# Optimization experiments

Measured on AMD Instinct MI355X. Metric: run time of the kernel, lower is better.

The kernel has to match this reference:

```python
import jax, jax.numpy as jnp
import numpy as np

G = 4096   # num_genes
P = 4096   # num_perts
H = 64     # hidden_size
B = 4      # num_graphs
E1 = 81920 # coexpress edges
E2 = 81920 # GO edges
FF = 512   # transformer ffn
NH = 2     # attention heads
INTER, LAT = 32, 16  # VAE dims

def _bn(x, g, b, eps=1e-5):
    # BatchNorm1d in training mode: batch stats (biased var)
    m = x.mean(0); v = x.var(0)
    return (x - m) / jnp.sqrt(v + eps) * g + b

def _ln(x, g, b, eps=1e-5):
    m = x.mean(-1, keepdims=True); v = x.var(-1, keepdims=True)
    return (x - m) / jnp.sqrt(v + eps) * g + b

def _mlp2(x, w1, b1, g1, be1, w2, b2, g2, be2):
    # MLP([a,b,c]) builds Linear->BN->ReLU->Linear->BN (trailing ReLU stripped)
    h = jax.nn.relu(_bn(x @ w1.T + b1, g1, be1))
    return _bn(h @ w2.T + b2, g2, be2)

def _sgconv(x, ei, ew, w, b, n):
    # SGConv K=1: gcn_norm (self loops, symmetric norm) then linear
    src = jnp.concatenate([ei[0], jnp.arange(n)])
    dst = jnp.concatenate([ei[1], jnp.arange(n)])
    wgt = jnp.concatenate([ew, jnp.ones((n,), ew.dtype)])
    deg = jax.ops.segment_sum(wgt, dst, num_segments=n)
    dinv = jnp.where(deg > 0, 1.0 / jnp.sqrt(jnp.where(deg > 0, deg, 1.0)), 0.0)
    norm = dinv[dst] * wgt * dinv[src]
    agg = jax.ops.segment_sum(norm[:, None] * x[src], dst, num_segments=n)
    return agg @ w.T + b

def setup_inputs():
    ks = iter(jax.random.split(jax.random.key(0), 80))
    def nrm(shape, s=0.05):
        return jax.random.normal(next(ks), shape, dtype=jnp.float32) * s
    d = {}
    d['x'] = jax.random.uniform(next(ks), (B * G,), dtype=jnp.float32)
    d['pert_idx'] = jax.random.randint(next(ks), (B, 2), 0, P)
    d['mask'] = jnp.zeros((G, G), jnp.float32)
    d['ei_co'] = jax.random.randint(next(ks), (2, E1), 0, G)
    d['w_co'] = jax.random.uniform(next(ks), (E1,), dtype=jnp.float32)
    d['ei_go'] = jax.random.randint(next(ks), (2, E2), 0, P)
    d['w_go'] = jax.random.uniform(next(ks), (E2,), dtype=jnp.float32)
    d['gene_emb'] = nrm((G, H)); d['emb_pos'] = nrm((G, H)); d['pert_tbl'] = nrm((P, H))
    d['sg_co_w'] = nrm((H, H)); d['sg_co_b'] = jnp.zeros((H,))
    d['sg_go_w'] = nrm((H, H)); d['sg_go_b'] = jnp.zeros((H,))
    d['bn_emb_g'] = jnp.ones((H,)); d['bn_emb_b'] = jnp.zeros((H,))
    for pre, din, dout in [('etv2_1', H, H), ('etv2_2', H, H), ('pf_1', H, H), ('pf_2', H, H), ('rw_1', H, 2 * H), ('rw_2', 2 * H, H)]:
        d[pre + '_w'] = nrm((dout, din)); d[pre + '_b'] = jnp.zeros((dout,))
        d[pre + '_g'] = jnp.ones((dout,)); d[pre + '_be'] = jnp.zeros((dout,))
    d['bnpb_g'] = jnp.ones((H,)); d['bnpb_b'] = jnp.zeros((H,))
    d['attn_in_w'] = nrm((3 * H, H)); d['attn_in_b'] = jnp.zeros((3 * H,))
    d['attn_out_w'] = nrm((H, H)); d['attn_out_b'] = jnp.zeros((H,))
    d['ln1_g'] = jnp.ones((H,)); d['ln1_b'] = jnp.zeros((H,))
    d['ff1_w'] = nrm((FF, H)); d['ff1_b'] = jnp.zeros((FF,))
    d['ff2_w'] = nrm((H, FF)); d['ff2_b'] = jnp.zeros((H,))
    d['ln2_g'] = jnp.ones((H,)); d['ln2_b'] = jnp.zeros((H,))
    d['indv_w1'] = nrm((G, H)); d['indv_b1'] = jnp.zeros((G,))
    d['vae_e1_w'] = nrm((INTER, G)); d['vae_e1_b'] = jnp.zeros((INTER,))
    d['vae_mu_w'] = nrm((LAT, INTER)); d['vae_mu_b'] = jnp.zeros((LAT,))
    d['vae_lv_w'] = nrm((LAT, INTER)); d['vae_lv_b'] = jnp.zeros((LAT,))
    d['vae_d1_w'] = nrm((INTER, LAT)); d['vae_d1_b'] = jnp.zeros((INTER,))
    d['vae_d2_w'] = nrm((G, INTER)); d['vae_d2_b'] = jnp.zeros((G,))
    d['eps'] = jax.random.normal(next(ks), (B, LAT), dtype=jnp.float32)
    return d

def reference(x, pert_idx, mask, ei_co, w_co, ei_go, w_go, gene_emb, emb_pos, pert_tbl, sg_co_w, sg_co_b, sg_go_w, sg_go_b, bn_emb_g, bn_emb_b, etv2_1_w, etv2_1_b, etv2_1_g, etv2_1_be, etv2_2_w, etv2_2_b, etv2_2_g, etv2_2_be, pf_1_w, pf_1_b, pf_1_g, pf_1_be, pf_2_w, pf_2_b, pf_2_g, pf_2_be, rw_1_w, rw_1_b, rw_1_g, rw_1_be, rw_2_w, rw_2_b, rw_2_g, rw_2_be, bnpb_g, bnpb_b, attn_in_w, attn_in_b, attn_out_w, attn_out_b, ln1_g, ln1_b, ff1_w, ff1_b, ff2_w, ff2_b, ln2_g, ln2_b, indv_w1, indv_b1, vae_e1_w, vae_e1_b, vae_mu_w, vae_mu_b, vae_lv_w, vae_lv_b, vae_d1_w, vae_d1_b, vae_d2_w, vae_d2_b, eps):
    # gene base embedding (identical across graphs until pert fusion)
    base = jax.nn.relu(_bn(gene_emb, bn_emb_g, bn_emb_b))               # [G,H]
    pos = _sgconv(emb_pos, ei_co, w_co, sg_co_w, sg_co_b, G)            # 1 gene-GNN layer
    base = base + 0.2 * pos
    base = _mlp2(base, etv2_1_w, etv2_1_b, etv2_1_g, etv2_1_be, etv2_2_w, etv2_2_b, etv2_2_g, etv2_2_be)
    # pert embeddings propagated on GO graph
    pge = _sgconv(pert_tbl, ei_go, w_go, sg_go_w, sg_go_b, P)           # [P,H]
    # per-graph pert_track: sum of pert embeddings (all pert_idx valid)
    psum = pge[pert_idx].sum(axis=1)                                    # [B,H]
    etot = _mlp2(psum, pf_1_w, pf_1_b, pf_1_g, pf_1_be, pf_2_w, pf_2_b, pf_2_g, pf_2_be)
    base_b = base[None, :, :] + etot[:, None, :]                        # [B,G,H]
    flat = jax.nn.relu(_bn(base_b.reshape(B * G, H), bnpb_g, bnpb_b))
    out = _mlp2(flat, rw_1_w, rw_1_b, rw_1_g, rw_1_be, rw_2_w, rw_2_b, rw_2_g, rw_2_be)
    out = out.reshape(B, G, H)
    # transformer encoder layer (post-norm, relu, nhead=2), eval/no-dropout
    qkv = out @ attn_in_w.T + attn_in_b
    q, k, v = jnp.split(qkv, 3, axis=-1)
    hd = H // NH
    q = q.reshape(B, G, NH, hd); k = k.reshape(B, G, NH, hd); v = v.reshape(B, G, NH, hd)
    sc = jnp.einsum('bqhd,bkhd->bhqk', q, k) / np.float32(np.sqrt(hd)) + mask
    a = jax.nn.softmax(sc, axis=-1)
    ctx = jnp.einsum('bhqk,bkhd->bqhd', a, v).reshape(B, G, H)
    att = ctx @ attn_out_w.T + attn_out_b
    h1 = _ln(out + att, ln1_g, ln1_b)
    ff = jax.nn.relu(h1 @ ff1_w.T + ff1_b) @ ff2_w.T + ff2_b
    enc = _ln(h1 + ff, ln2_g, ln2_b)
    # per-gene linear: (enc.unsqueeze(-1)*indv_w1).sum(2)+indv_b1
    pred0 = jnp.einsum('bgh,gh->bg', enc, indv_w1) + indv_b1
    # VAE branch on raw expression
    xr = x.reshape(B, G)
    he = jax.nn.relu(xr @ vae_e1_w.T + vae_e1_b)
    mu = he @ vae_mu_w.T + vae_mu_b
    lv = he @ vae_lv_w.T + vae_lv_b
    z = mu + eps * jnp.exp(0.5 * lv)
    hdc = jax.nn.relu(z @ vae_d1_w.T + vae_d1_b)
    recon = hdc @ vae_d2_w.T + vae_d2_b
    kl = -0.5 * jnp.mean(jnp.sum(1.0 + lv - mu ** 2 - jnp.exp(lv), axis=1))
    recon = jnp.where(xr == 0, 0.0, recon)
    pred = pred0 + recon
    return (pred, kl)
```

## Files before the change

### kernel.cpp

```cpp
#include <hip/hip_runtime.h>
#include <hip/hip_bf16.h>
#include <math.h>

#define GG 4096
#define PP 4096
#define HH 64
#define BB 4
#define E1N 81920
#define E2N 81920
#define FFD 512
#define BNEPS 1e-5f
#define LOG2E 1.44269504088896341f
#define QPRE (0.17677669529663687f * LOG2E)

typedef unsigned short ushort_t;
typedef unsigned int uint_t;
using sh8 = __attribute__((ext_vector_type(8))) short;
using sh4 = __attribute__((ext_vector_type(4))) short;
using f4  = __attribute__((ext_vector_type(4))) float;

struct MaskOn  { static constexpr bool v = true; };
struct MaskOff { static constexpr bool v = false; };

#if __has_builtin(__builtin_amdgcn_mfma_f32_16x16x16bf16_1k)
#define MFMA16(a, b, c) __builtin_amdgcn_mfma_f32_16x16x16bf16_1k((a), (b), (c), 0, 0, 0)
#elif __has_builtin(__builtin_amdgcn_mfma_f32_16x16x16_bf16)
#define MFMA16(a, b, c) __builtin_amdgcn_mfma_f32_16x16x16_bf16((a), (b), (c), 0, 0, 0)
#else
static __device__ inline f4 mfma16_asm(sh4 a, sh4 b, f4 c) {
    f4 d;
    asm volatile("v_mfma_f32_16x16x16_bf16 %0, %1, %2, %3"
                 : "=v"(d) : "v"(a), "v"(b), "v"(c));
    return d;
}
#define MFMA16(a, b, c) mfma16_asm((a), (b), (c))
#endif

#define OF_STATS   0
#define OF_DEGCO   2048
#define OF_DEGGO   6144
#define OF_PSLOT   10240
#define OF_ETOT    10752
#define OF_HDC     11008
#define OF_HE      11136
#define OF_MFLAG   11264
#define OF_CNT     12288
#define OF_OFFS    16384
#define OF_WOFF    20608
#define OF_SSRC    24704
#define OF_SNRM    106624
#define OF_BASEIN  274432
#define OF_Y1      536576
#define OF_Y2      798720
#define OF_FLAT    1060864
#define OF_RW1     2109440
#define OF_RW2     4206592
#define OF_OUT     5255168
#define OF_QKV     6303744
#define OF_QB      12288
#define OF_KB      (OF_QB + 524288)
#define OF_VF      OF_FLAT
#define OF_OPA     OF_QKV
#define OF_OPB     OF_OUT
#define OF_LP      OF_RW1
#define OPS        1048576
#define OF_W1B     9449472
#define OF_W2B     9465856

__device__ inline ushort_t f2b(float f) {
    uint_t u = __builtin_bit_cast(uint_t, f);
    u += 0x7FFFu + ((u >> 16) & 1u);
    return (ushort_t)(u >> 16);
}

__device__ inline void gld16(const void* gptr, void* lptr) {
    __builtin_amdgcn_global_load_lds(
        (const __attribute__((address_space(1))) uint_t*)gptr,
        (__attribute__((address_space(3))) uint_t*)lptr, 16, 0, 0);
}

__device__ void dev_vae_he(int bid, const float* __restrict__ x, const float* __restrict__ W,
                           const float* __restrict__ bias, float* he, float* sh) {
    int b = bid >> 5, i = bid & 31;
    float s = 0.f;
    for (int g = threadIdx.x; g < 4096; g += 256) s += x[b * 4096 + g] * W[i * 4096 + g];
    sh[threadIdx.x] = s;
    __syncthreads();
    for (int o = 128; o > 0; o >>= 1) {
        if (threadIdx.x < o) sh[threadIdx.x] += sh[threadIdx.x + o];
        __syncthreads();
    }
    if (threadIdx.x == 0) he[b * 32 + i] = fmaxf(sh[0] + bias[i], 0.f);
}

__device__ void dev_vae_mid(const float* __restrict__ he,
                            const float* __restrict__ muw, const float* __restrict__ mub,
                            const float* __restrict__ lvw, const float* __restrict__ lvb,
                            const float* __restrict__ d1w, const float* __restrict__ d1b,
                            const float* __restrict__ eps, float* hdc, float* klout, float* zs) {
    int t = threadIdx.x;
    if (t < 64) {
        int b = t >> 4, l = t & 15;
        float mu = mub[l], lv = lvb[l];
        for (int i = 0; i < 32; i++) {
            float hv = he[b * 32 + i];
            mu += hv * muw[l * 32 + i];
            lv += hv * lvw[l * 32 + i];
        }
        zs[t] = mu + eps[t] * expf(0.5f * lv);
        float kterm = 1.f + lv - mu * mu - expf(lv);
        for (int o = 32; o > 0; o >>= 1) kterm += __shfl_xor(kterm, o, 64);
        if (t == 0) klout[0] = -0.5f * kterm * 0.25f;
    }
    __syncthreads();
    if (t < 128) {
        int b = t >> 5, i = t & 31;
        float a = d1b[i];
        for (int l = 0; l < 16; l++) a += zs[b * 16 + l] * d1w[i * 16 + l];
        hdc[t] = fmaxf(a, 0.f);
    }
}

__device__ void dev_edge_deg(int bid, const int* __restrict__ ei, const float* __restrict__ w,
                             float* deg, int E, int* cnt) {
    int e = bid * 256 + threadIdx.x;
    if (e < E) {
        int d = ei[E + e];
        atomicAdd(&deg[d], w[e]);
        if (cnt) atomicAdd(&cnt[d], 1);
    }
}

__device__ void dev_cs_part(int bid, const float* __restrict__ X, int N,
                            float* sum, float* sumsq, float* sh) {
    int t = threadIdx.x;
    int col = t & 63, ro = t >> 6;
    int rows = N >> 8;
    int r0 = bid * rows;
    float s = 0.f, q = 0.f;
    for (int r = r0 + ro; r < r0 + rows; r += 4) {
        float v = X[r * 64 + col];
        s += v; q += v * v;
    }
    float* ls = sh; float* lq = sh + 256;
    ls[t] = s; lq[t] = q;
    __syncthreads();
    if (t < 64) {
        for (int j = t + 64; j < 256; j += 64) { s += ls[j]; q += lq[j]; }
        atomicAdd(&sum[t], s);
        atomicAdd(&sumsq[t], q);
    }
}

__device__ void dev_mask_scan(int bid, const float* __restrict__ mask, int* flag) {
    const uint4* m4 = (const uint4*)mask;
    const int total = (GG * GG) / 4;
    uint_t acc = 0u;
    for (int i = bid * 256 + threadIdx.x; i < total; i += 512 * 256) {
        uint4 v = m4[i];
        acc |= v.x | v.y | v.z | v.w;
    }
    if (acc) atomicOr(flag, 1);
}

__device__ void dev_scatter(int bid, const int* __restrict__ ei, const float* __restrict__ w,
                            const float* __restrict__ deg,
                            int* woff, int* ssrc, float* snrm) {
    int e = bid * 256 + threadIdx.x;
    if (e >= E1N) return;
    int src = ei[e], dst = ei[E1N + e];
    float nrm = rsqrtf(deg[dst] + 1.f) * w[e] * rsqrtf(deg[src] + 1.f);
    int pos = atomicAdd(&woff[dst], 1);
    ssrc[pos] = src;
    snrm[pos] = nrm;
}

__device__ void dev_pert_edges(int bid, const int* __restrict__ pidx, const int* __restrict__ ei,
                               const float* __restrict__ w, const float* __restrict__ deg,
                               const float* __restrict__ tbl, float* pslot) {
    int e = bid * 256 + threadIdx.x;
    int lane = threadIdx.x & 63;
    bool valid = e < E2N;
    int dst = valid ? ei[E2N + e] : -1;
    int hit = 0;
    #pragma unroll
    for (int s = 0; s < 8; s++) hit |= (pidx[s] == dst) ? (1 << s) : 0;
    if (__ballot(hit != 0) == 0) return;
    int src = valid ? ei[e] : 0;
    float nrm = 0.f;
    if (hit) nrm = rsqrtf(deg[dst] + 1.f) * w[e] * rsqrtf(deg[src] + 1.f);
    for (int s = 0; s < 8; s++) {
        unsigned long long m = __ballot((hit >> s) & 1);
        while (m) {
            int l = __builtin_ctzll(m);
            m &= m - 1;
            int es = __shfl(src, l, 64);
            float en = __shfl(nrm, l, 64);
            atomicAdd(&pslot[s * 64 + lane], en * tbl[es * 64 + lane]);
        }
    }
}

__device__ void dev_base_combine(int bid, const float* __restrict__ gene_emb,
                                 const int* __restrict__ off, const int* __restrict__ ssrc,
                                 const float* __restrict__ snrm,
                                 const float* __restrict__ emb_pos,
                                 const float* __restrict__ deg,
                                 const float* __restrict__ W, const float* __restrict__ bias,
                                 const float* __restrict__ bsum, const float* __restrict__ bsq,
                                 const float* __restrict__ bg, const float* __restrict__ bb,
                                 float* out, float* sh) {
    float* Wt = sh;
    float* a = sh + 4160;
    int t = threadIdx.x;
    for (int i = t; i < 4096; i += 256) Wt[(i & 63) * 65 + (i >> 6)] = W[i];
    int rr = t >> 6, h = t & 63;
    int g = bid * 4 + rr;
    float acc = emb_pos[g * 64 + h] / (deg[g] + 1.f);
    int e = off[g];
    const int e1 = off[g + 1];
    for (; e + 4 <= e1; e += 4) {
        int s0 = ssrc[e], s1 = ssrc[e + 1], s2 = ssrc[e + 2], s3 = ssrc[e + 3];
        float n0 = snrm[e], n1 = snrm[e + 1], n2 = snrm[e + 2], n3 = snrm[e + 3];
        acc += n0 * emb_pos[s0 * 64 + h];
        acc += n1 * emb_pos[s1 * 64 + h];
        acc += n2 * emb_pos[s2 * 64 + h];
        acc += n3 * emb_pos[s3 * 64 + h];
    }
    for (; e < e1; e++) acc += snrm[e] * emb_pos[ssrc[e] * 64 + h];
    a[rr * 64 + h] = acc;
    __syncthreads();
    float y = bias[h];
    const float* ar = a + rr * 64;
    #pragma unroll 8
    for (int k = 0; k < 64; k++) y += ar[k] * Wt[k * 65 + h];
    const float invN = 1.0f / (float)GG;
    float m = bsum[h] * invN;
    float is_ = rsqrtf(bsq[h] * invN - m * m + BNEPS);
    float v = gene_emb[g * 64 + h];
    v = (v - m) * is_ * bg[h] + bb[h];
    v = fmaxf(v, 0.f);
    out[g * 64 + h] = v + 0.2f * y;
}

__device__ void dev_pert_mlp(const float* __restrict__ pslot, const int* __restrict__ pidx,
                             const float* __restrict__ deg, const float* __restrict__ tbl,
                             const float* __restrict__ gw, const float* __restrict__ gb,
                             const float* __restrict__ w1, const float* __restrict__ b1,
                             const float* __restrict__ g1, const float* __restrict__ be1,
                             const float* __restrict__ w2, const float* __restrict__ b2,
                             const float* __restrict__ g2, const float* __restrict__ be2,
                             float* etot, float* sh) {
    float* pge = sh;
    float* psum = sh + 512;
    float* y = sh + 768;
    float* mh = sh + 1024;
    float* ih = sh + 1088;
    int t = threadIdx.x;
    for (int j = t; j < 512; j += 256) {
        int s = j >> 6, h = j & 63;
        int n = pidx[s];
        float invd = 1.0f / (deg[n] + 1.f);
        float acc = gb[h];
        for (int k = 0; k < 64; k++)
            acc += (pslot[s * 64 + k] + tbl[n * 64 + k] * invd) * gw[h * 64 + k];
        pge[j] = acc;
    }
    __syncthreads();
    { int b = t >> 6, h = t & 63; psum[t] = pge[2 * b * 64 + h] + pge[(2 * b + 1) * 64 + h]; }
    __syncthreads();
    { int h = t & 63; int b = t >> 6;
      float acc = b1[h];
      for (int k = 0; k < 64; k++) acc += psum[b * 64 + k] * w1[h * 64 + k];
      y[t] = acc; }
    __syncthreads();
    if (t < 64) {
        float s = 0.f, sq = 0.f;
        for (int b = 0; b < 4; b++) { float v = y[b * 64 + t]; s += v; sq += v * v; }
        float m = s * 0.25f;
        mh[t] = m; ih[t] = rsqrtf(sq * 0.25f - m * m + BNEPS);
    }
    __syncthreads();
    { int h = t & 63;
      float v = (y[t] - mh[h]) * ih[h] * g1[h] + be1[h];
      psum[t] = fmaxf(v, 0.f); }
    __syncthreads();
    { int h = t & 63; int b = t >> 6;
      float acc = b2[h];
      for (int k = 0; k < 64; k++) acc += psum[b * 64 + k] * w2[h * 64 + k];
      y[t] = acc; }
    __syncthreads();
    if (t < 64) {
        float s = 0.f, sq = 0.f;
        for (int b = 0; b < 4; b++) { float v = y[b * 64 + t]; s += v; sq += v * v; }
        float m = s * 0.25f;
        mh[t] = m; ih[t] = rsqrtf(sq * 0.25f - m * m + BNEPS);
    }
    __syncthreads();
    { int h = t & 63;
      etot[t] = (y[t] - mh[h]) * ih[h] * g2[h] + be2[h]; }
}

__global__ void k_fat12(float* ws, const int* __restrict__ ei_co, const float* __restrict__ w_co,
                        const int* __restrict__ ei_go, const float* __restrict__ w_go,
                        const float* __restrict__ gene_emb, const float* __restrict__ x,
                        const float* __restrict__ ve1_w, const float* __restrict__ ve1_b,
                        const float* __restrict__ ff1_w, const float* __restrict__ ff2_w,
                        const float* __restrict__ mask) {
    __shared__ float sh[512];
    int bid = blockIdx.x;
    if (bid < 320) dev_edge_deg(bid, ei_co, w_co, ws + OF_DEGCO, E1N, (int*)(ws + OF_CNT));
    else if (bid < 640) dev_edge_deg(bid - 320, ei_go, w_go, ws + OF_DEGGO, E2N, nullptr);
    else if (bid < 896) dev_cs_part(bid - 640, gene_emb, GG, ws + OF_STATS, ws + OF_STATS + 128, sh);
    else if (bid < 1024) dev_vae_he(bid - 896, x, ve1_w, ve1_b, ws + OF_HE, sh);
    else if (bid < 1280) {
        int i = (bid - 1024) * 256 + threadIdx.x;
        ushort_t* W1b = (ushort_t*)(ws + OF_W1B);
        ushort_t* W2b = (ushort_t*)(ws + OF_W2B);
        if (i < 32768) W1b[i] = f2b(ff1_w[i]);
        else W2b[i - 32768] = f2b(ff2_w[i - 32768]);
    } else dev_mask_scan(bid - 1280, mask, (int*)(ws + OF_MFLAG));
}

__global__ void k_scan(float* ws) {
    int* cnt = (int*)(ws + OF_CNT);
    int* off = (int*)(ws + OF_OFFS);
    int* woff = (int*)(ws + OF_WOFF);
    __shared__ int part[256];
    const int t = threadIdx.x;
    int loc[16];
    int s = 0;
    #pragma unroll
    for (int i = 0; i < 16; i++) { loc[i] = s; s += cnt[t * 16 + i]; }
    part[t] = s;
    __syncthreads();
    for (int o = 1; o < 256; o <<= 1) {
        int v = (t >= o) ? part[t - o] : 0;
        __syncthreads();
        part[t] += v;
        __syncthreads();
    }
    int prev = (t == 0) ? 0 : part[t - 1];
    #pragma unroll
    for (int i = 0; i < 16; i++) {
        int o = prev + loc[i];
        off[t * 16 + i] = o;
        woff[t * 16 + i] = o;
    }
    if (t == 255) off[4096] = part[255];
}

__global__ void k_fat3(float* ws, const int* __restrict__ ei_co, const float* __restrict__ w_co,
                       const int* __restrict__ pidx,
                       const int* __restrict__ ei_go, const float* __restrict__ w_go,
                       const float* __restrict__ pert_tbl,
                       const float* __restrict__ vmu_w, const float* __restrict__ vmu_b,
                       const float* __restrict__ vlv_w, const float* __restrict__ vlv_b,
                       const float* __restrict__ vd1_w, const float* __restrict__ vd1_b,
                       const float* __restrict__ veps, float* klout) {
    __shared__ float sh[512];
    int bid = blockIdx.x;
    if (bid < 320)
        dev_scatter(bid, ei_co, w_co, ws + OF_DEGCO,
                    (int*)(ws + OF_WOFF), (int*)(ws + OF_SSRC), ws + OF_SNRM);
    else if (bid < 640)
        dev_pert_edges(bid - 320, pidx, ei_go, w_go, ws + OF_DEGGO, pert_tbl, ws + OF_PSLOT);
    else dev_vae_mid(ws + OF_HE, vmu_w, vmu_b, vlv_w, vlv_b, vd1_w, vd1_b, veps,
                     ws + OF_HDC, klout, sh);
}

__global__ void k_fat4(float* ws, const float* __restrict__ gene_emb,
                       const float* __restrict__ emb_pos,
                       const float* __restrict__ sg_co_w, const float* __restrict__ sg_co_b,
                       const float* __restrict__ bn_emb_g, const float* __restrict__ bn_emb_b,
                       const int* __restrict__ pidx, const float* __restrict__ pert_tbl,
                       const float* __restrict__ gw, const float* __restrict__ gb,
                       const float* __restrict__ w1, const float* __restrict__ b1,
                       const float* __restrict__ g1, const float* __restrict__ be1,
                       const float* __restrict__ w2, const float* __restrict__ b2,
                       const float* __restrict__ g2, const float* __restrict__ be2) {
    __shared__ float sh[4416];
    int bid = blockIdx.x;
    if (bid < 1024)
        dev_base_combine(bid, gene_emb, (const int*)(ws + OF_OFFS),
                         (const int*)(ws + OF_SSRC), ws + OF_SNRM,
                         emb_pos, ws + OF_DEGCO,
                         sg_co_w, sg_co_b, ws + OF_STATS, ws + OF_STATS + 128,
                         bn_emb_g, bn_emb_b, ws + OF_BASEIN, sh);
    else
        dev_pert_mlp(ws + OF_PSLOT, pidx, ws + OF_DEGGO, pert_tbl, gw, gb,
                     w1, b1, g1, be1, w2, b2, g2, be2, ws + OF_ETOT, sh);
}

__launch_bounds__(256)
__global__ void k_gemm64(const float* __restrict__ X, const float* __restrict__ W,
                         const float* __restrict__ bias, float* __restrict__ Y,
                         int Cin, int Cout,
                         const float* __restrict__ bnsum, const float* __restrict__ bnsq,
                         const float* __restrict__ bng, const float* __restrict__ bnb,
                         float invN, int relu_in,
                         float* __restrict__ outsum, float* __restrict__ outsq) {
    __shared__ float Xs[64][66];
    __shared__ float Ws[64][66];
    __shared__ float bsc[64], bsh[64];
    const int t = threadIdx.x;
    const int row0 = blockIdx.x * 64, cb = blockIdx.y * 64;
    const int tx = t & 15, ty = t >> 4;
    const int c0 = tx * 4, r0 = ty * 4;
    float acc[4][4];
    #pragma unroll
    for (int j = 0; j < 4; j++)
        #pragma unroll
        for (int i = 0; i < 4; i++) acc[j][i] = 0.f;

    for (int k0 = 0; k0 < Cin; k0 += 64) {
        __syncthreads();
        if (t < 64) {
            float sc = 1.f, sh = 0.f;
            if (bnsum) {
                int c = k0 + t;
                float m = bnsum[c] * invN;
                float is_ = rsqrtf(bnsq[c] * invN - m * m + BNEPS);
                sc = is_ * bng[c]; sh = bnb[c] - m * sc;
            }
            bsc[t] = sc; bsh[t] = sh;
        }
        __syncthreads();
        for (int i = t; i < 1024; i += 256) {
            int r = i >> 4, kq = (i & 15) * 4;
            float4 v = *(const float4*)&X[(size_t)(row0 + r) * Cin + k0 + kq];
            float e0 = v.x * bsc[kq] + bsh[kq];
            float e1 = v.y * bsc[kq + 1] + bsh[kq + 1];
            float e2 = v.z * bsc[kq + 2] + bsh[kq + 2];
            float e3 = v.w * bsc[kq + 3] + bsh[kq + 3];
            if (relu_in) {
                e0 = fmaxf(e0, 0.f); e1 = fmaxf(e1, 0.f);
                e2 = fmaxf(e2, 0.f); e3 = fmaxf(e3, 0.f);
            }
            Xs[r][kq] = e0; Xs[r][kq + 1] = e1; Xs[r][kq + 2] = e2; Xs[r][kq + 3] = e3;
            float4 wv = *(const float4*)&W[(size_t)(cb + r) * Cin + k0 + kq];
            Ws[r][kq] = wv.x; Ws[r][kq + 1] = wv.y; Ws[r][kq + 2] = wv.z; Ws[r][kq + 3] = wv.w;
        }
        __syncthreads();
        #pragma unroll 4
        for (int k = 0; k < 64; k += 2) {
            float2 a[4], b[4];
            #pragma unroll
            for (int j = 0; j < 4; j++) a[j] = *(const float2*)&Xs[r0 + j][k];
            #pragma unroll
            for (int i = 0; i < 4; i++) b[i] = *(const float2*)&Ws[c0 + i][k];
            #pragma unroll
            for (int j = 0; j < 4; j++)
                #pragma unroll
                for (int i = 0; i < 4; i++)
                    acc[j][i] += a[j].x * b[i].x + a[j].y * b[i].y;
        }
    }
    float4 bi = *(const float4*)&bias[cb + c0];
    float scol[4] = {0.f, 0.f, 0.f, 0.f}, qcol[4] = {0.f, 0.f, 0.f, 0.f};
    #pragma unroll
    for (int j = 0; j < 4; j++) {
        float4 o;
        o.x = acc[j][0] + bi.x; o.y = acc[j][1] + bi.y;
        o.z = acc[j][2] + bi.z; o.w = acc[j][3] + bi.w;
        *(float4*)&Y[(size_t)(row0 + r0 + j) * Cout + cb + c0] = o;
        scol[0] += o.x; scol[1] += o.y; scol[2] += o.z; scol[3] += o.w;
        qcol[0] += o.x * o.x; qcol[1] += o.y * o.y;
        qcol[2] += o.z * o.z; qcol[3] += o.w * o.w;
    }
    if (outsum) {
        __syncthreads();
        #pragma unroll
        for (int i = 0; i < 4; i++) { Xs[ty][c0 + i] = scol[i]; Ws[ty][c0 + i] = qcol[i]; }
        __syncthreads();
        if (t < 64) {
            float ss = 0.f, qq = 0.f;
            #pragma unroll
            for (int r = 0; r < 16; r++) { ss += Xs[r][t]; qq += Ws[r][t]; }
            atomicAdd(&outsum[cb + t], ss);
            atomicAdd(&outsq[cb + t], qq);
        }
    }
}

__launch_bounds__(256)
__global__ void k_gemm_rw1(const float* __restrict__ y2, const float* __restrict__ etot,
                           const float* __restrict__ s2sum, const float* __restrict__ s2sq,
                           const float* __restrict__ g2e, const float* __restrict__ b2e,
                           const float* __restrict__ g3, const float* __restrict__ b3,
                           const float* __restrict__ W, const float* __restrict__ bias,
                           float* __restrict__ Y,
                           float* __restrict__ osum, float* __restrict__ osq) {
    __shared__ float Xs[64][66];
    __shared__ float Ws[64][66];
    __shared__ float bsc[64], bsh[64];
    const int t = threadIdx.x;
    const int row0 = blockIdx.x * 64, cb = blockIdx.y * 64;
    const int tx = t & 15, ty = t >> 4;
    const int c0 = tx * 4, r0 = ty * 4;
    const int bb = row0 >> 12;
    if (t < 64) {
        const float iG = 1.0f / 4096.f, iNG = 1.0f / 16384.f;
        float S1 = s2sum[t], S2 = s2sq[t];
        float m2 = S1 * iG;
        float is2 = rsqrtf(S2 * iG - m2 * m2 + BNEPS);
        float sc2 = is2 * g2e[t], sh2 = b2e[t] - m2 * sc2;
        float sz = sc2 * S1 + 4096.f * sh2;
        float szz = sc2 * sc2 * S2 + 2.f * sc2 * sh2 * S1 + 4096.f * sh2 * sh2;
        float e0 = etot[t], e1 = etot[64 + t], e2 = etot[128 + t], e3 = etot[192 + t];
        float se = e0 + e1 + e2 + e3;
        float see = e0 * e0 + e1 * e1 + e2 * e2 + e3 * e3;
        float sumF = 4.f * sz + 4096.f * se;
        float sqF = 4.f * szz + 2.f * sz * se + 4096.f * see;
        float m3 = sumF * iNG;
        float is3 = rsqrtf(sqF * iNG - m3 * m3 + BNEPS);
        float eb = etot[bb * 64 + t];
        bsc[t] = sc2 * is3 * g3[t];
        bsh[t] = (sh2 + eb - m3) * is3 * g3[t] + b3[t];
    }
    __syncthreads();
    for (int i = t; i < 1024; i += 256) {
        int r = i >> 4, kq = (i & 15) * 4;
        int g = (row0 + r) & 4095;
        float4 v = *(const float4*)&y2[(size_t)g * 64 + kq];
        Xs[r][kq] = fmaxf(v.x * bsc[kq] + bsh[kq], 0.f);
        Xs[r][kq + 1] = fmaxf(v.y * bsc[kq + 1] + bsh[kq + 1], 0.f);
        Xs[r][kq + 2] = fmaxf(v.z * bsc[kq + 2] + bsh[kq + 2], 0.f);
        Xs[r][kq + 3] = fmaxf(v.w * bsc[kq + 3] + bsh[kq + 3], 0.f);
        float4 wv = *(const float4*)&W[(size_t)(cb + r) * 64 + kq];
        Ws[r][kq] = wv.x; Ws[r][kq + 1] = wv.y; Ws[r][kq + 2] = wv.z; Ws[r][kq + 3] = wv.w;
    }
    __syncthreads();
    float acc[4][4];
    #pragma unroll
    for (int j = 0; j < 4; j++)
        #pragma unroll
        for (int i = 0; i < 4; i++) acc[j][i] = 0.f;
    #pragma unroll 4
    for (int k = 0; k < 64; k += 2) {
        float2 a[4], b[4];
        #pragma unroll
        for (int j = 0; j < 4; j++) a[j] = *(const float2*)&Xs[r0 + j][k];
        #pragma unroll
        for (int i = 0; i < 4; i++) b[i] = *(const float2*)&Ws[c0 + i][k];
        #pragma unroll
        for (int j = 0; j < 4; j++)
            #pragma unroll
            for (int i = 0; i < 4; i++)
                acc[j][i] += a[j].x * b[i].x + a[j].y * b[i].y;
    }
    float4 bi = *(const float4*)&bias[cb + c0];
    float scol[4] = {0.f, 0.f, 0.f, 0.f}, qcol[4] = {0.f, 0.f, 0.f, 0.f};
    #pragma unroll
    for (int j = 0; j < 4; j++) {
        float4 o;
        o.x = acc[j][0] + bi.x; o.y = acc[j][1] + bi.y;
        o.z = acc[j][2] + bi.z; o.w = acc[j][3] + bi.w;
        *(float4*)&Y[(size_t)(row0 + r0 + j) * 128 + cb + c0] = o;
        scol[0] += o.x; scol[1] += o.y; scol[2] += o.z; scol[3] += o.w;
        qcol[0] += o.x * o.x; qcol[1] += o.y * o.y;
        qcol[2] += o.z * o.z; qcol[3] += o.w * o.w;
    }
    __syncthreads();
    #pragma unroll
    for (int i = 0; i < 4; i++) { Xs[ty][c0 + i] = scol[i]; Ws[ty][c0 + i] = qcol[i]; }
    __syncthreads();
    if (t < 64) {
        float ss = 0.f, qq = 0.f;
        #pragma unroll
        for (int r = 0; r < 16; r++) { ss += Xs[r][t]; qq += Ws[r][t]; }
        atomicAdd(&osum[cb + t], ss);
        atomicAdd(&osq[cb + t], qq);
    }
}

__launch_bounds__(256)
__global__ void k_gemm_qkv(const float* __restrict__ X, const float* __restrict__ W,
                           const float* __restrict__ bias,
                           const float* __restrict__ bnsum, const float* __restrict__ bnsq,
                           const float* __restrict__ bng, const float* __restrict__ bnb,
                           ushort_t* __restrict__ Qb, ushort_t* __restrict__ Kb,
                           ushort_t* __restrict__ Vf) {
    __shared__ float Xs[64][66];
    __shared__ float Ws[64][66];
    __shared__ float bsc[64], bsh[64];
    const int t = threadIdx.x;
    const int row0 = blockIdx.x * 64, yb = blockIdx.y, cb = yb * 64;
    const int tx = t & 15, ty = t >> 4;
    const int c0 = tx * 4, r0 = ty * 4;
    const float invN = 1.0f / (float)(BB * GG);
    if (t < 64) {
        float m = bnsum[t] * invN;
        float is_ = rsqrtf(bnsq[t] * invN - m * m + BNEPS);
        float sc = is_ * bng[t];
        bsc[t] = sc; bsh[t] = bnb[t] - m * sc;
    }
    __syncthreads();
    for (int i = t; i < 1024; i += 256) {
        int r = i >> 4, kq = (i & 15) * 4;
        float4 v = *(const float4*)&X[(size_t)(row0 + r) * 64 + kq];
        Xs[r][kq] = v.x * bsc[kq] + bsh[kq];
        Xs[r][kq + 1] = v.y * bsc[kq + 1] + bsh[kq + 1];
        Xs[r][kq + 2] = v.z * bsc[kq + 2] + bsh[kq + 2];
        Xs[r][kq + 3] = v.w * bsc[kq + 3] + bsh[kq + 3];
        float4 wv = *(const float4*)&W[(size_t)(cb + r) * 64 + kq];
        Ws[r][kq] = wv.x; Ws[r][kq + 1] = wv.y; Ws[r][kq + 2] = wv.z; Ws[r][kq + 3] = wv.w;
    }
    __syncthreads();
    float acc[4][4];
    #pragma unroll
    for (int j = 0; j < 4; j++)
        #pragma unroll
        for (int i = 0; i < 4; i++) acc[j][i] = 0.f;
    #pragma unroll 4
    for (int k = 0; k < 64; k += 2) {
        float2 a[4], b[4];
        #pragma unroll
        for (int j = 0; j < 4; j++) a[j] = *(const float2*)&Xs[r0 + j][k];
        #pragma unroll
        for (int i = 0; i < 4; i++) b[i] = *(const float2*)&Ws[c0 + i][k];
        #pragma unroll
        for (int j = 0; j < 4; j++)
            #pragma unroll
            for (int i = 0; i < 4; i++)
                acc[j][i] += a[j].x * b[i].x + a[j].y * b[i].y;
    }
    float4 bi = *(const float4*)&bias[cb + c0];
    const int b2 = row0 >> 12, tile = (row0 & 4095) >> 6;
    if (yb < 2) {
        ushort_t* Dst = (yb == 0) ? Qb : Kb;
        const float sc2 = (yb == 0) ? QPRE : 1.0f;
        const int h = c0 >> 5, d = c0 & 31;
        #pragma unroll
        for (int j = 0; j < 4; j++) {
            union { ushort_t u[4]; uint2 v; } pk;
            pk.u[0] = f2b((acc[j][0] + bi.x) * sc2);
            pk.u[1] = f2b((acc[j][1] + bi.y) * sc2);
            pk.u[2] = f2b((acc[j][2] + bi.z) * sc2);
            pk.u[3] = f2b((acc[j][3] + bi.w) * sc2);
            int g = (row0 & 4095) + r0 + j;
            *(uint2*)&Dst[((size_t)(b2 * 2 + h) * GG + g) * 32 + d] = pk.v;
        }
    } else {
        __syncthreads();
        #pragma unroll
        for (int j = 0; j < 4; j++) {
            Xs[r0 + j][c0] = acc[j][0] + bi.x;
            Xs[r0 + j][c0 + 1] = acc[j][1] + bi.y;
            Xs[r0 + j][c0 + 2] = acc[j][2] + bi.z;
            Xs[r0 + j][c0 + 3] = acc[j][3] + bi.w;
        }
        __syncthreads();
        #pragma unroll
        for (int h = 0; h < 2; h++) {
            union { ushort_t u[8]; uint4 v; } pk;
            #pragma unroll
            for (int j = 0; j < 8; j++) {
                int idx = t * 8 + j;
                int g2 = idx >> 8, L = (idx >> 2) & 63, i = idx & 3;
                int key = (g2 >> 1) * 16 + ((L >> 4) << 2) + i;
                int d = ((g2 & 1) << 4) + (L & 15);
                pk.u[j] = f2b(Xs[key][h * 32 + d]);
            }
            *(uint4*)&Vf[((size_t)((b2 * 2 + h) * 64 + tile)) * 2048 + t * 8] = pk.v;
        }
    }
}

__launch_bounds__(512, 4)
__global__ void k_attn_mfma(const ushort_t* __restrict__ Qb, const ushort_t* __restrict__ Kb,
                            const ushort_t* __restrict__ Vf, const float* __restrict__ mask,
                            const float* __restrict__ mflag,
                            float* __restrict__ opA, float* __restrict__ opB,
                            float* __restrict__ Lp) {
    __shared__ ushort_t Kl[2][2][4096];
    __shared__ ushort_t Vl[2][2][4096];
    const int split = blockIdx.y;
    const int bh0 = blockIdx.z * 2;
    const int q0 = blockIdx.x * 64;
    const int kstart = split * (GG / 2), kend = kstart + (GG / 2);
    const int t = threadIdx.x;
    const int lane = t & 63, w = t >> 6;
    const int qg = w >> 1, kh = w & 1;
    const int l15 = lane & 15, quad = lane >> 4;
    const int um = (*(const int*)mflag) != 0;

    sh8 qf[2];
    #pragma unroll
    for (int bh = 0; bh < 2; bh++)
        qf[bh] = *(const sh8*)&Qb[((size_t)(bh0 + bh) * GG + q0 + qg * 16 + l15) * 32 + quad * 8];
    const float* mrow = mask + (size_t)(q0 + qg * 16 + l15) * GG + quad * 4;

    auto stage = [&](int buf, int k0) {
        int bh = t >> 8, c = t & 255;
        int key = ((c >> 6) << 4) + (c & 15);
        int chunk = (c >> 4) & 3;
        #pragma unroll
        for (int s = 0; s < 2; s++) {
            gld16(Kb + ((size_t)(bh0 + bh) * GG + k0 + s * 64 + key) * 32 + chunk * 8,
                  &Kl[buf][bh][s * 2048 + c * 8]);
            gld16(Vf + ((size_t)((bh0 + bh) * 64 + (k0 >> 6) + s)) * 2048 + c * 8,
                  &Vl[buf][bh][s * 2048 + c * 8]);
        }
    };
    stage(0, kstart);

    f4 O0[2], O1[2];
    float ls[2];
    #pragma unroll
    for (int bh = 0; bh < 2; bh++) {
        O0[bh] = f4{0.f, 0.f, 0.f, 0.f};
        O1[bh] = f4{0.f, 0.f, 0.f, 0.f};
        ls[bh] = 0.f;
    }

    auto run = [&](auto tag) {
        constexpr bool U = decltype(tag)::v;
        for (int k0 = kstart; k0 < kend; k0 += 128) {
            const int cur = ((k0 - kstart) >> 7) & 1;
            __syncthreads();
            if (k0 + 128 < kend) stage(cur ^ 1, k0 + 128);
            #pragma unroll
            for (int bh = 0; bh < 2; bh++) {
                #pragma unroll
                for (int ii = 0; ii < 4; ii++) {
                    const int i2 = kh * 4 + ii;
                    sh8 kf = *(const sh8*)&Kl[cur][bh][(i2 * 64 + lane) * 8];
                    f4 z = {0.f, 0.f, 0.f, 0.f};
                    f4 sa = __builtin_amdgcn_mfma_f32_16x16x32_bf16(kf, qf[bh], z, 0, 0, 0);
                    float p0, p1, p2, p3;
                    if constexpr (U) {
                        float4 mv = *(const float4*)&mrow[k0 + i2 * 16];
                        p0 = exp2f(fmaf(mv.x, LOG2E, sa[0]));
                        p1 = exp2f(fmaf(mv.y, LOG2E, sa[1]));
                        p2 = exp2f(fmaf(mv.z, LOG2E, sa[2]));
                        p3 = exp2f(fmaf(mv.w, LOG2E, sa[3]));
                    } else {
                        p0 = exp2f(sa[0]); p1 = exp2f(sa[1]);
                        p2 = exp2f(sa[2]); p3 = exp2f(sa[3]);
                    }
                    ls[bh] += (p0 + p1) + (p2 + p3);
                    union { __hip_bfloat162 h2[2]; sh4 v; } pkp;
                    pkp.h2[0] = __float22bfloat162_rn(float2{p0, p1});
                    pkp.h2[1] = __float22bfloat162_rn(float2{p2, p3});
                    sh4 vf0 = *(const sh4*)&Vl[cur][bh][((i2 * 2 + 0) * 64 + lane) * 4];
                    sh4 vf1 = *(const sh4*)&Vl[cur][bh][((i2 * 2 + 1) * 64 + lane) * 4];
                    O0[bh] = MFMA16(pkp.v, vf0, O0[bh]);
                    O1[bh] = MFMA16(pkp.v, vf1, O1[bh]);
                }
            }
        }
    };
    if (um) run(MaskOn{}); else run(MaskOff{});

    #pragma unroll
    for (int bh = 0; bh < 2; bh++) {
        ls[bh] += __shfl_xor(ls[bh], 16, 64);
        ls[bh] += __shfl_xor(ls[bh], 32, 64);
    }
    __syncthreads();
    float* Ox = (float*)&Kl[0][0][0];
    float* Lx = (float*)&Vl[0][0][0];
    if (kh == 0) {
        #pragma unroll
        for (int bh = 0; bh < 2; bh++) {
            #pragma unroll
            for (int r = 0; r < 4; r++) {
                int ql = qg * 16 + quad * 4 + r;
                Ox[(bh * 64 + ql) * 32 + l15] = O0[bh][r];
                Ox[(bh * 64 + ql) * 32 + l15 + 16] = O1[bh][r];
            }
            if (quad == 0) Lx[bh * 64 + qg * 16 + l15] = ls[bh];
        }
    }
    __syncthreads();
    if (kh == 1) {
        float* op = (split == 0) ? opA : opB;
        #pragma unroll
        for (int bh = 0; bh < 2; bh++) {
            int gbh = bh0 + bh;
            #pragma unroll
            for (int r = 0; r < 4; r++) {
                int ql = qg * 16 + quad * 4 + r;
                size_t o = ((size_t)gbh * GG + q0 + ql) * 32 + l15;
                op[o] = O0[bh][r] + Ox[(bh * 64 + ql) * 32 + l15];
                op[o + 16] = O1[bh][r] + Ox[(bh * 64 + ql) * 32 + l15 + 16];
            }
            if (quad == 0)
                Lp[split * 32768 + gbh * GG + q0 + qg * 16 + l15] =
                    ls[bh] + Lx[bh * 64 + qg * 16 + l15];
        }
    }
}

__launch_bounds__(256)
__global__ void k_tail(const float* __restrict__ opA, const float* __restrict__ opB,
                       const float* __restrict__ Lp, const float* __restrict__ yrw2,
                       const float* __restrict__ Waout, const float* __restrict__ baout,
                       const float* __restrict__ bsum5, const float* __restrict__ bsq5,
                       const float* __restrict__ bg5, const float* __restrict__ bb5,
                       const float* __restrict__ lg1, const float* __restrict__ lb1,
                       const ushort_t* __restrict__ W1b, const float* __restrict__ b1f,
                       const ushort_t* __restrict__ W2b, const float* __restrict__ b2f,
                       const float* __restrict__ lg2, const float* __restrict__ lb2,
                       const float* __restrict__ indvw, const float* __restrict__ indvb,
                       const float* __restrict__ hdc, const float* __restrict__ d2w,
                       const float* __restrict__ d2b, const float* __restrict__ x,
                       float* __restrict__ outp) {
    __shared__ float Wt[4160];
    __shared__ float Cs[4160];
    __shared__ ushort_t Hb[4096];
    __shared__ ushort_t FT[32768];
    __shared__ ushort_t WS[2][4096];
    const int t = threadIdx.x;
    const int r0b = blockIdx.x * 64;
    const int lane = t & 63, w = t >> 6;
    const int l15 = lane & 15, quad = lane >> 4;

    for (int i = t; i < 4096; i += 256) Wt[(i & 63) * 65 + (i >> 6)] = Waout[i];
    {
        int col = t & 63, rl = t >> 6;
        int hh = col >> 5, d = col & 31;
        for (int jj = 0; jj < 16; jj++) {
            int lrow = rl + jj * 4;
            int row = r0b + lrow;
            int b = row >> 12, q = row & 4095;
            int bhq = (b * 2 + hh) * GG + q;
            size_t oi = (size_t)bhq * 32 + d;
            float num = opA[oi] + opB[oi];
            float den = Lp[bhq] + Lp[32768 + bhq];
            Cs[lrow * 65 + col] = num / den;
        }
    }
    __syncthreads();
    const float invN = 1.0f / (float)(BB * GG);
    float m5 = bsum5[lane] * invN;
    float is5 = rsqrtf(bsq5[lane] * invN - m5 * m5 + BNEPS);
    float h1v[16];
    for (int j = 0; j < 16; j++) {
        int lrow = w * 16 + j;
        int row = r0b + lrow;
        float acc = baout[lane];
        const float* cr = Cs + lrow * 65;
        #pragma unroll 8
        for (int k = 0; k < 64; k++) acc += cr[k] * Wt[k * 65 + lane];
        float ov = (yrw2[(size_t)row * 64 + lane] - m5) * is5 * bg5[lane] + bb5[lane];
        float v = ov + acc;
        float s = v;
        for (int o = 32; o > 0; o >>= 1) s += __shfl_xor(s, o, 64);
        float mean = s * (1.f / 64.f);
        float d = v - mean;
        float sq = d * d;
        for (int o = 32; o > 0; o >>= 1) sq += __shfl_xor(sq, o, 64);
        float inv = rsqrtf(sq * (1.f / 64.f) + BNEPS);
        h1v[j] = d * inv * lg1[lane] + lb1[lane];
    }
    __syncthreads();
    float* h1f = Wt;
    for (int j = 0; j < 16; j++) h1f[(w * 16 + j) * 65 + lane] = h1v[j];
    __syncthreads();
    if (t < 128) {
        int kt = t >> 6, lane6 = t & 63;
        int q2 = (lane6 >> 4) & 3, r15 = lane6 & 15;
        for (int rg = 0; rg < 4; rg++) {
            union { ushort_t u[8]; uint4 v4; } pk;
            #pragma unroll
            for (int j = 0; j < 8; j++)
                pk.u[j] = f2b(h1f[(rg * 16 + r15) * 65 + kt * 32 + q2 * 8 + j]);
            *(uint4*)&Hb[(rg * 2 + kt) * 512 + lane6 * 8] = pk.v4;
        }
    }
    auto stage1 = [&](int buf, int cb8) {
        int cb = cb8 * 64;
        #pragma unroll
        for (int kt = 0; kt < 2; kt++)
            gld16(W1b + (size_t)((cb + w * 16 + l15) * 64 + kt * 32 + quad * 8),
                  &WS[buf][(w * 2 + kt) * 512 + lane * 8]);
    };
    stage1(0, 0);
    for (int cb8 = 0; cb8 < 8; cb8++) {
        const int cur = cb8 & 1;
        __syncthreads();
        if (cb8 + 1 < 8) stage1(cur ^ 1, cb8 + 1);
        sh8 xf0 = *(const sh8*)&Hb[(w * 2 + 0) * 512 + lane * 8];
        sh8 xf1 = *(const sh8*)&Hb[(w * 2 + 1) * 512 + lane * 8];
        const int cb = cb8 * 64;
        #pragma unroll
        for (int c = 0; c < 4; c++) {
            sh8 wf0 = *(const sh8*)&WS[cur][(c * 2 + 0) * 512 + lane * 8];
            sh8 wf1 = *(const sh8*)&WS[cur][(c * 2 + 1) * 512 + lane * 8];
            f4 z = {0.f, 0.f, 0.f, 0.f};
            f4 acc = __builtin_amdgcn_mfma_f32_16x16x32_bf16(wf0, xf0, z, 0, 0, 0);
            acc = __builtin_amdgcn_mfma_f32_16x16x32_bf16(wf1, xf1, acc, 0, 0, 0);
            float4 bv = *(const float4*)&b1f[cb + c * 16 + quad * 4];
            union { ushort_t u[4]; uint2 v2; } pk;
            pk.u[0] = f2b(fmaxf(acc[0] + bv.x, 0.f));
            pk.u[1] = f2b(fmaxf(acc[1] + bv.y, 0.f));
            pk.u[2] = f2b(fmaxf(acc[2] + bv.z, 0.f));
            pk.u[3] = f2b(fmaxf(acc[3] + bv.w, 0.f));
            int kt512 = cb8 * 2 + (c >> 1);
            int quadp = (c & 1) * 2 + (quad >> 1);
            int j0 = (quad & 1) * 4;
            *(uint2*)&FT[((w * 16 + kt512) * 64 + quadp * 16 + l15) * 8 + j0] = pk.v2;
        }
    }
    auto stage2 = [&](int buf, int k0) {
        #pragma unroll
        for (int kt = 0; kt < 2; kt++)
            gld16(W2b + (size_t)((w * 16 + l15) * 512 + k0 + kt * 32 + quad * 8),
                  &WS[buf][(w * 2 + kt) * 512 + lane * 8]);
    };
    stage2(0, 0);
    f4 acc2[4];
    #pragma unroll
    for (int c = 0; c < 4; c++) acc2[c] = f4{0.f, 0.f, 0.f, 0.f};
    for (int k0 = 0; k0 < 512; k0 += 64) {
        const int cur = (k0 >> 6) & 1;
        __syncthreads();
        if (k0 + 64 < 512) stage2(cur ^ 1, k0 + 64);
        const int ktb = k0 >> 5;
        #pragma unroll
        for (int kt = 0; kt < 2; kt++) {
            sh8 xf = *(const sh8*)&FT[((w * 16 + ktb + kt) * 64 + lane) * 8];
            #pragma unroll
            for (int c = 0; c < 4; c++) {
                sh8 wf = *(const sh8*)&WS[cur][(c * 2 + kt) * 512 + lane * 8];
                acc2[c] = __builtin_amdgcn_mfma_f32_16x16x32_bf16(wf, xf, acc2[c], 0, 0, 0);
            }
        }
    }
    const int row = r0b + w * 16 + l15;
    const int b = row >> 12, g = row & 4095;
    float v[4][4];
    float s = 0.f, sq = 0.f;
    #pragma unroll
    for (int c = 0; c < 4; c++) {
        float4 bv = *(const float4*)&b2f[c * 16 + quad * 4];
        #pragma unroll
        for (int i = 0; i < 4; i++) {
            float hv = h1f[(w * 16 + l15) * 65 + c * 16 + quad * 4 + i];
            float bvi = (i == 0) ? bv.x : (i == 1) ? bv.y : (i == 2) ? bv.z : bv.w;
            v[c][i] = hv + acc2[c][i] + bvi;
            s += v[c][i]; sq += v[c][i] * v[c][i];
        }
    }
    s += __shfl_xor(s, 16, 64);  s += __shfl_xor(s, 32, 64);
    sq += __shfl_xor(sq, 16, 64); sq += __shfl_xor(sq, 32, 64);
    float mean = s * (1.f / 64.f);
    float inv = rsqrtf(sq * (1.f / 64.f) - mean * mean + BNEPS);
    float pd = 0.f;
    #pragma unroll
    for (int c = 0; c < 4; c++) {
        float4 lgv = *(const float4*)&lg2[c * 16 + quad * 4];
        float4 lbv = *(const float4*)&lb2[c * 16 + quad * 4];
        float4 iwv = *(const float4*)&indvw[(size_t)g * 64 + c * 16 + quad * 4];
        pd += ((v[c][0] - mean) * inv * lgv.x + lbv.x) * iwv.x;
        pd += ((v[c][1] - mean) * inv * lgv.y + lbv.y) * iwv.y;
        pd += ((v[c][2] - mean) * inv * lgv.z + lbv.z) * iwv.z;
        pd += ((v[c][3] - mean) * inv * lgv.w + lbv.w) * iwv.w;
    }
    float rc = 0.f;
    #pragma unroll
    for (int i = 0; i < 8; i++)
        rc += hdc[b * 32 + quad * 8 + i] * d2w[(size_t)g * 32 + quad * 8 + i];
    pd += __shfl_xor(pd, 16, 64); pd += __shfl_xor(pd, 32, 64);
    rc += __shfl_xor(rc, 16, 64); rc += __shfl_xor(rc, 32, 64);
    if (quad == 0) {
        float recon = rc + d2b[g];
        if (x[row] == 0.f) recon = 0.f;
        outp[row] = pd + indvb[g] + recon;
    }
}

extern "C" void kernel_launch(void* const* d_in, const int* in_sizes, int n_in,
                              void* d_out, int out_size, void* d_ws, size_t ws_size,
                              hipStream_t stream) {
    const float* x        = (const float*)d_in[0];
    const int*   pert_idx = (const int*)  d_in[1];
    const float* mask     = (const float*)d_in[2];
    const int*   ei_co    = (const int*)  d_in[3];
    const float* w_co     = (const float*)d_in[4];
    const int*   ei_go    = (const int*)  d_in[5];
    const float* w_go     = (const float*)d_in[6];
    const float* gene_emb = (const float*)d_in[7];
    const float* emb_pos  = (const float*)d_in[8];
    const float* pert_tbl = (const float*)d_in[9];
    const float* sg_co_w  = (const float*)d_in[10];
    const float* sg_co_b  = (const float*)d_in[11];
    const float* sg_go_w  = (const float*)d_in[12];
    const float* sg_go_b  = (const float*)d_in[13];
    const float* bn_emb_g = (const float*)d_in[14];
    const float* bn_emb_b = (const float*)d_in[15];
    const float* etv1_w   = (const float*)d_in[16];
    const float* etv1_b   = (const float*)d_in[17];
    const float* etv1_g   = (const float*)d_in[18];
    const float* etv1_be  = (const float*)d_in[19];
    const float* etv2_w   = (const float*)d_in[20];
    const float* etv2_b   = (const float*)d_in[21];
    const float* etv2_g   = (const float*)d_in[22];
    const float* etv2_be  = (const float*)d_in[23];
    const float* pf1_w    = (const float*)d_in[24];
    const float* pf1_b    = (const float*)d_in[25];
    const float* pf1_g    = (const float*)d_in[26];
    const float* pf1_be   = (const float*)d_in[27];
    const float* pf2_w    = (const float*)d_in[28];
    const float* pf2_b    = (const float*)d_in[29];
    const float* pf2_g    = (const float*)d_in[30];
    const float* pf2_be   = (const float*)d_in[31];
    const float* rw1_w    = (const float*)d_in[32];
    const float* rw1_b    = (const float*)d_in[33];
    const float* rw1_g    = (const float*)d_in[34];
    const float* rw1_be   = (const float*)d_in[35];
    const float* rw2_w    = (const float*)d_in[36];
    const float* rw2_b    = (const float*)d_in[37];
    const float* rw2_g    = (const float*)d_in[38];
    const float* rw2_be   = (const float*)d_in[39];
    const float* bnpb_g   = (const float*)d_in[40];
    const float* bnpb_b   = (const float*)d_in[41];
    const float* ain_w    = (const float*)d_in[42];
    const float* ain_b    = (const float*)d_in[43];
    const float* aout_w   = (const float*)d_in[44];
    const float* aout_b   = (const float*)d_in[45];
    const float* ln1_g    = (const float*)d_in[46];
    const float* ln1_b    = (const float*)d_in[47];
    const float* ff1_w    = (const float*)d_in[48];
    const float* ff1_b    = (const float*)d_in[49];
    const float* ff2_w    = (const float*)d_in[50];
    const float* ff2_b    = (const float*)d_in[51];
    const float* ln2_g    = (const float*)d_in[52];
    const float* ln2_b    = (const float*)d_in[53];
    const float* indv_w   = (const float*)d_in[54];
    const float* indv_b   = (const float*)d_in[55];
    const float* ve1_w    = (const float*)d_in[56];
    const float* ve1_b    = (const float*)d_in[57];
    const float* vmu_w    = (const float*)d_in[58];
    const float* vmu_b    = (const float*)d_in[59];
    const float* vlv_w    = (const float*)d_in[60];
    const float* vlv_b    = (const float*)d_in[61];
    const float* vd1_w    = (const float*)d_in[62];
    const float* vd1_b    = (const float*)d_in[63];
    const float* vd2_w    = (const float*)d_in[64];
    const float* vd2_b    = (const float*)d_in[65];
    const float* veps     = (const float*)d_in[66];

    float* ws   = (float*)d_ws;
    float* outp = (float*)d_out;

    float* stm1 = ws + OF_STATS + 1 * 256; float* sti1 = stm1 + 128;
    float* stm2 = ws + OF_STATS + 2 * 256; float* sti2 = stm2 + 128;
    float* stm4 = ws + OF_STATS + 4 * 256; float* sti4 = stm4 + 128;
    float* stm5 = ws + OF_STATS + 5 * 256; float* sti5 = stm5 + 128;

    float* basein = ws + OF_BASEIN;
    float* y1     = ws + OF_Y1;
    float* y2     = ws + OF_Y2;
    float* yrw1   = ws + OF_RW1;
    float* yrw2   = ws + OF_RW2;
    float* opA    = ws + OF_OPA;
    float* opB    = ws + OF_OPB;
    float* Lp     = ws + OF_LP;
    ushort_t* Qb  = (ushort_t*)(ws + OF_QB);
    ushort_t* Kb  = (ushort_t*)(ws + OF_KB);
    ushort_t* Vf  = (ushort_t*)(ws + OF_VF);
    ushort_t* W1b = (ushort_t*)(ws + OF_W1B);
    ushort_t* W2b = (ushort_t*)(ws + OF_W2B);

    const int NG = BB * GG;
    const float iG = 1.0f / (float)GG, iNG = 1.0f / (float)NG;

    hipMemsetAsync(ws, 0, 11268 * sizeof(float), stream);
    hipMemsetAsync(ws + OF_CNT, 0, 4096 * sizeof(int), stream);

    k_fat12<<<1792, 256, 0, stream>>>(ws, ei_co, w_co, ei_go, w_go, gene_emb,
                                      x, ve1_w, ve1_b, ff1_w, ff2_w, mask);
    k_scan<<<1, 256, 0, stream>>>(ws);
    k_fat3<<<641, 256, 0, stream>>>(ws, ei_co, w_co, pert_idx,
                                    ei_go, w_go, pert_tbl,
                                    vmu_w, vmu_b, vlv_w, vlv_b, vd1_w, vd1_b,
                                    veps, outp + NG);
    k_fat4<<<1025, 256, 0, stream>>>(ws, gene_emb, emb_pos, sg_co_w, sg_co_b,
                                     bn_emb_g, bn_emb_b, pert_idx, pert_tbl,
                                     sg_go_w, sg_go_b,
                                     pf1_w, pf1_b, pf1_g, pf1_be,
                                     pf2_w, pf2_b, pf2_g, pf2_be);
    k_gemm64<<<dim3(GG / 64, 1), 256, 0, stream>>>(basein, etv1_w, etv1_b, y1, 64, 64,
                                                   nullptr, nullptr, nullptr, nullptr, 0.f, 0,
                                                   stm1, sti1);
    k_gemm64<<<dim3(GG / 64, 1), 256, 0, stream>>>(y1, etv2_w, etv2_b, y2, 64, 64,
                                                   stm1, sti1, etv1_g, etv1_be, iG, 1,
                                                   stm2, sti2);
    k_gemm_rw1<<<dim3(NG / 64, 2), 256, 0, stream>>>(y2, ws + OF_ETOT, stm2, sti2,
                                                     etv2_g, etv2_be, bnpb_g, bnpb_b,
                                                     rw1_w, rw1_b, yrw1, stm4, sti4);
    k_gemm64<<<dim3(NG / 64, 1), 256, 0, stream>>>(yrw1, rw2_w, rw2_b, yrw2, 128, 64,
                                                   stm4, sti4, rw1_g, rw1_be, iNG, 1,
                                                   stm5, sti5);
    k_gemm_qkv<<<dim3(NG / 64, 3), 256, 0, stream>>>(yrw2, ain_w, ain_b,
                                                     stm5, sti5, rw2_g, rw2_be,
                                                     Qb, Kb, Vf);
    k_attn_mfma<<<dim3(GG / 64, 2, 4), 512, 0, stream>>>(Qb, Kb, Vf, mask,
                                                         ws + OF_MFLAG, opA, opB, Lp);
    k_tail<<<NG / 64, 256, 0, stream>>>(opA, opB, Lp, yrw2, aout_w, aout_b,
                                        stm5, sti5, rw2_g, rw2_be, ln1_g, ln1_b,
                                        W1b, ff1_b, W2b, ff2_b, ln2_g, ln2_b,
                                        indv_w, indv_b, ws + OF_HDC, vd2_w, vd2_b,
                                        x, outp);
}
```

Measured before the change: 445.7 us.

## Split tail kernel into attention-combine and FFN kernels for more parallelism

```diff
diff --git a/kernel.cpp b/kernel.cpp
--- a/kernel.cpp
+++ b/kernel.cpp
@@ -63,6 +63,7 @@
 #define OF_OPA     OF_QKV
 #define OF_OPB     OF_OUT
 #define OF_LP      OF_RW1
+#define OF_H1      (OF_RW1 + 131072)
 #define OPS        1048576
 #define OF_W1B     9449472
 #define OF_W2B     9465856
@@ -794,35 +795,25 @@
 }
 
 __launch_bounds__(256)
-__global__ void k_tail(const float* __restrict__ opA, const float* __restrict__ opB,
+__global__ void k_comb(const float* __restrict__ opA, const float* __restrict__ opB,
                        const float* __restrict__ Lp, const float* __restrict__ yrw2,
                        const float* __restrict__ Waout, const float* __restrict__ baout,
                        const float* __restrict__ bsum5, const float* __restrict__ bsq5,
                        const float* __restrict__ bg5, const float* __restrict__ bb5,
                        const float* __restrict__ lg1, const float* __restrict__ lb1,
-                       const ushort_t* __restrict__ W1b, const float* __restrict__ b1f,
-                       const ushort_t* __restrict__ W2b, const float* __restrict__ b2f,
-                       const float* __restrict__ lg2, const float* __restrict__ lb2,
-                       const float* __restrict__ indvw, const float* __restrict__ indvb,
-                       const float* __restrict__ hdc, const float* __restrict__ d2w,
-                       const float* __restrict__ d2b, const float* __restrict__ x,
-                       float* __restrict__ outp) {
+                       float* __restrict__ h1out) {
     __shared__ float Wt[4160];
-    __shared__ float Cs[4160];
-    __shared__ ushort_t Hb[4096];
-    __shared__ ushort_t FT[32768];
-    __shared__ ushort_t WS[2][4096];
+    __shared__ float Cs[1040];
     const int t = threadIdx.x;
-    const int r0b = blockIdx.x * 64;
+    const int r0b = blockIdx.x * 16;
     const int lane = t & 63, w = t >> 6;
-    const int l15 = lane & 15, quad = lane >> 4;
-
     for (int i = t; i < 4096; i += 256) Wt[(i & 63) * 65 + (i >> 6)] = Waout[i];
     {
         int col = t & 63, rl = t >> 6;
         int hh = col >> 5, d = col & 31;
-        for (int jj = 0; jj < 16; jj++) {
-            int lrow = rl + jj * 4;
+        #pragma unroll
+        for (int jj = 0; jj < 4; jj++) {
+            int lrow = rl * 4 + jj;
             int row = r0b + lrow;
             int b = row >> 12, q = row & 4095;
             int bhq = (b * 2 + hh) * GG + q;
@@ -836,9 +827,9 @@
     const float invN = 1.0f / (float)(BB * GG);
     float m5 = bsum5[lane] * invN;
     float is5 = rsqrtf(bsq5[lane] * invN - m5 * m5 + BNEPS);
-    float h1v[16];
-    for (int j = 0; j < 16; j++) {
-        int lrow = w * 16 + j;
+    #pragma unroll
+    for (int j = 0; j < 4; j++) {
+        int lrow = w * 4 + j;
         int row = r0b + lrow;
         float acc = baout[lane];
         const float* cr = Cs + lrow * 65;
@@ -853,20 +844,37 @@
         float sq = d * d;
         for (int o = 32; o > 0; o >>= 1) sq += __shfl_xor(sq, o, 64);
         float inv = rsqrtf(sq * (1.f / 64.f) + BNEPS);
-        h1v[j] = d * inv * lg1[lane] + lb1[lane];
-    }
-    __syncthreads();
-    float* h1f = Wt;
-    for (int j = 0; j < 16; j++) h1f[(w * 16 + j) * 65 + lane] = h1v[j];
-    __syncthreads();
+        h1out[(size_t)row * 64 + lane] = d * inv * lg1[lane] + lb1[lane];
+    }
+}
+
+__launch_bounds__(256)
+__global__ void k_ffn(const float* __restrict__ h1,
+                      const ushort_t* __restrict__ W1b, const float* __restrict__ b1f,
+                      const ushort_t* __restrict__ W2b, const float* __restrict__ b2f,
+                      const float* __restrict__ lg2, const float* __restrict__ lb2,
+                      const float* __restrict__ indvw, const float* __restrict__ indvb,
+                      const float* __restrict__ hdc, const float* __restrict__ d2w,
+                      const float* __restrict__ d2b, const float* __restrict__ x,
+                      float* __restrict__ outp) {
+    __shared__ ushort_t Hb[4096];
+    __shared__ ushort_t FT[32768];
+    __shared__ ushort_t WS[2][4096];
+    const int t = threadIdx.x;
+    const int r0b = blockIdx.x * 64;
+    const int lane = t & 63, w = t >> 6;
+    const int l15 = lane & 15, quad = lane >> 4;
+
     if (t < 128) {
         int kt = t >> 6, lane6 = t & 63;
         int q2 = (lane6 >> 4) & 3, r15 = lane6 & 15;
         for (int rg = 0; rg < 4; rg++) {
+            const float* hrow = &h1[(size_t)(r0b + rg * 16 + r15) * 64 + kt * 32 + q2 * 8];
+            float4 v0 = *(const float4*)&hrow[0];
+            float4 v1 = *(const float4*)&hrow[4];
             union { ushort_t u[8]; uint4 v4; } pk;
-            #pragma unroll
-            for (int j = 0; j < 8; j++)
-                pk.u[j] = f2b(h1f[(rg * 16 + r15) * 65 + kt * 32 + q2 * 8 + j]);
+            pk.u[0] = f2b(v0.x); pk.u[1] = f2b(v0.y); pk.u[2] = f2b(v0.z); pk.u[3] = f2b(v0.w);
+            pk.u[4] = f2b(v1.x); pk.u[5] = f2b(v1.y); pk.u[6] = f2b(v1.z); pk.u[7] = f2b(v1.w);
             *(uint4*)&Hb[(rg * 2 + kt) * 512 + lane6 * 8] = pk.v4;
         }
     }
@@ -936,9 +944,10 @@
     #pragma unroll
     for (int c = 0; c < 4; c++) {
         float4 bv = *(const float4*)&b2f[c * 16 + quad * 4];
+        float4 hv4 = *(const float4*)&h1[(size_t)row * 64 + c * 16 + quad * 4];
         #pragma unroll
         for (int i = 0; i < 4; i++) {
-            float hv = h1f[(w * 16 + l15) * 65 + c * 16 + quad * 4 + i];
+            float hv = (i == 0) ? hv4.x : (i == 1) ? hv4.y : (i == 2) ? hv4.z : hv4.w;
             float bvi = (i == 0) ? bv.x : (i == 1) ? bv.y : (i == 2) ? bv.z : bv.w;
             v[c][i] = hv + acc2[c][i] + bvi;
             s += v[c][i]; sq += v[c][i] * v[c][i];
@@ -1059,6 +1068,7 @@
     float* opA    = ws + OF_OPA;
     float* opB    = ws + OF_OPB;
     float* Lp     = ws + OF_LP;
+    float* h1buf  = ws + OF_H1;
     ushort_t* Qb  = (ushort_t*)(ws + OF_QB);
     ushort_t* Kb  = (ushort_t*)(ws + OF_KB);
     ushort_t* Vf  = (ushort_t*)(ws + OF_VF);
@@ -1100,9 +1110,9 @@
                                                      Qb, Kb, Vf);
     k_attn_mfma<<<dim3(GG / 64, 2, 4), 512, 0, stream>>>(Qb, Kb, Vf, mask,
                                                          ws + OF_MFLAG, opA, opB, Lp);
-    k_tail<<<NG / 64, 256, 0, stream>>>(opA, opB, Lp, yrw2, aout_w, aout_b,
-                                        stm5, sti5, rw2_g, rw2_be, ln1_g, ln1_b,
-                                        W1b, ff1_b, W2b, ff2_b, ln2_g, ln2_b,
-                                        indv_w, indv_b, ws + OF_HDC, vd2_w, vd2_b,
-                                        x, outp);
-}
+    k_comb<<<NG / 16, 256, 0, stream>>>(opA, opB, Lp, yrw2, aout_w, aout_b,
+                                        stm5, sti5, rw2_g, rw2_be, ln1_g, ln1_b, h1buf);
+    k_ffn<<<NG / 64, 256, 0, stream>>>(h1buf, W1b, ff1_b, W2b, ff2_b, ln2_g, ln2_b,
+                                       indv_w, indv_b, ws + OF_HDC, vd2_w, vd2_b,
+                                       x, outp);
+}
```

Result: no change. 440.3 us (-1.2%).
